# Performance work log

Hardware: AMD Instinct MI355X
Metric: run time of the kernel (lower is better)

The kernel has to match this reference:

```python
import jax, jax.numpy as jnp
import numpy as np

INPUT_SIZE = 512
HIDDEN = 512
LAYERS = 4
T = 256
B = 64


def _weight_size():
    total = 0
    for l in range(LAYERS):
        insize = INPUT_SIZE if l == 0 else HIDDEN
        total += insize * 6 * HIDDEN + HIDDEN * 5 * HIDDEN
    return total


def setup_inputs() -> dict:
    key = jax.random.key(0)
    k1, k2, k3 = jax.random.split(key, 3)
    inputs = jax.random.normal(k1, (B, T, INPUT_SIZE), dtype=jnp.float32)
    lengths = jax.random.randint(k2, (B,), T // 2, T + 1)
    lengths = jnp.sort(lengths)[::-1].astype(jnp.int32)  # descending, like pack_padded
    weight = jax.random.normal(k3, (_weight_size(),), dtype=jnp.float32) * 0.05
    # bias: zeros except forget-gate block (second of 5) filled with 1, per layer
    b_layer = jnp.concatenate([
        jnp.zeros((HIDDEN,), jnp.float32),
        jnp.ones((HIDDEN,), jnp.float32),
        jnp.zeros((3 * HIDDEN,), jnp.float32),
    ])
    bias = jnp.tile(b_layer, LAYERS)
    return {"inputs": inputs, "weight": weight, "bias": bias, "lengths": lengths}


def _split_params(weight, bias):
    params = []
    idx = 0
    for l in range(LAYERS):
        insize = INPUT_SIZE if l == 0 else HIDDEN
        n = insize * 6 * HIDDEN
        W_ih = weight[idx:idx + n].reshape(insize, 6 * HIDDEN); idx += n
        n = HIDDEN * 5 * HIDDEN
        W_hh = weight[idx:idx + n].reshape(HIDDEN, 5 * HIDDEN); idx += n
        b = bias[l * 5 * HIDDEN:(l + 1) * 5 * HIDDEN]
        params.append((W_ih, W_hh, b))
    return params


def _reverse_padded(x, lengths):
    # x: [T, B, D]; reverse each sequence within its own length, keep padding in place
    t = jnp.arange(x.shape[0])[:, None]                      # [T, 1]
    L = lengths[None, :]                                     # [1, B]
    idx = jnp.where(t < L, L - 1 - t, t)                     # [T, B]
    return jnp.take_along_axis(x, idx[:, :, None], axis=0)


def _run_layer(x, W_ih, W_hh, b, mask):
    # x: [T, B, D], mask: [T, B, 1] (1.0 where t < length)
    H = HIDDEN
    xi = jnp.einsum('tbd,dg->tbg', x, W_ih)                  # [T, B, 6H] (batched GEMM)

    def step(carry, inp):
        h, c = carry
        xi_t, m = inp
        g = xi_t[:, :5 * H] + h @ W_hh + b                   # [B, 5H]
        i = jax.nn.sigmoid(g[:, 0 * H:1 * H])
        f = jax.nn.sigmoid(g[:, 1 * H:2 * H])
        gc = jnp.tanh(g[:, 2 * H:3 * H])
        o = jax.nn.sigmoid(g[:, 3 * H:4 * H])
        r = jax.nn.sigmoid(g[:, 4 * H:5 * H])                # highway transform gate
        lin = xi_t[:, 5 * H:]                                # highway linear projection of input
        c_new = (f * c + i * gc) * m
        h_new = (r * (o * jnp.tanh(c_new)) + (1.0 - r) * lin) * m
        return (h_new, c_new), h_new

    h0 = jnp.zeros((x.shape[1], H), x.dtype)
    (_, _), hs = jax.lax.scan(step, (h0, h0), (xi, mask))
    return hs                                                # [T, B, H]


def reference(inputs, weight, bias, lengths):
    x = jnp.transpose(inputs, (1, 0, 2))                     # [T, B, D]
    mask = (jnp.arange(T)[:, None] < lengths[None, :]).astype(x.dtype)[:, :, None]
    x = x * mask                                             # emulate packed-sequence zero padding
    for l, (W_ih, W_hh, b) in enumerate(_split_params(weight, bias)):
        rev = (l % 2 == 1)                                   # layers alternate direction
        if rev:
            x = _reverse_padded(x, lengths)
        h = _run_layer(x, W_ih, W_hh, b, mask)
        if rev:
            h = _reverse_padded(h, lengths)
        x = h
    return jnp.transpose(x, (1, 0, 2))                       # [B, T, H]
```

## Files before the change

### kernel.cpp

```cpp
#include <hip/hip_runtime.h>
#include <hip/hip_bf16.h>

#define T_STEPS 256
#define BATCH 64
#define HID 512
#define GATES 3072
#define NLAYERS 4
#define BT_GROUPS 4
#define GBLK 32
#define SCAN_THREADS 256
#define HSTR 520
#define GLP 84

typedef __bf16 bf16_t;
typedef _Float16 fp16_t;
typedef __attribute__((ext_vector_type(8))) __bf16 bf16x8;
typedef __attribute__((ext_vector_type(4))) float f32x4;
typedef __attribute__((ext_vector_type(4))) unsigned int u32x4;

__device__ __forceinline__ float sigm(float x){ return 1.0f/(1.0f + __expf(-x)); }
__device__ __forceinline__ float tanh_f(float x){ return 2.0f/(1.0f + __expf(-2.0f*x)) - 1.0f; }
__device__ __forceinline__ unsigned short f2bf(float x){ __bf16 b=(__bf16)x; return __builtin_bit_cast(unsigned short, b); }

__global__ void transpose_cast_kernel(const float* __restrict__ src, unsigned short* __restrict__ dst, int R, int C){
  __shared__ float tile[32][33];
  int tx = threadIdx.x & 31, ty = threadIdx.x >> 5;
  int c0 = blockIdx.x*32, r0 = blockIdx.y*32;
  #pragma unroll
  for(int i=0;i<4;i++){ int r = r0 + ty + i*8; tile[ty+i*8][tx] = src[(size_t)r*C + c0 + tx]; }
  __syncthreads();
  #pragma unroll
  for(int i=0;i<4;i++){ int c = c0 + ty + i*8; dst[(size_t)c*R + r0 + tx] = f2bf(tile[tx][ty+i*8]); }
}

__global__ void prep_x0_kernel(const float* __restrict__ inp, const int* __restrict__ lens, unsigned short* __restrict__ x0){
  int idx = blockIdx.x*blockDim.x + threadIdx.x;
  int e = idx*4;
  int d = e & (HID-1);
  int tb = e >> 9;
  int b = tb & (BATCH-1);
  int t = tb >> 6;
  const float4 v = *(const float4*)(inp + ((size_t)b*T_STEPS + t)*HID + d);
  float m = (t < lens[b]) ? 1.f : 0.f;
  ushort4 u; u.x=f2bf(v.x*m); u.y=f2bf(v.y*m); u.z=f2bf(v.z*m); u.w=f2bf(v.w*m);
  *(ushort4*)(x0 + ((size_t)t*BATCH + b)*HID + d) = u;
}

__global__ void __launch_bounds__(256,2)
xi_gemm_kernel(const unsigned short* __restrict__ A,
               const unsigned short* __restrict__ BT,
               fp16_t* __restrict__ C)
{
  __shared__ __align__(16) unsigned short As[128*72];
  __shared__ __align__(16) unsigned short Bs[128*72];
  const int tid = threadIdx.x, lane = tid & 63, wv = tid >> 6;
  const int frow = lane & 15, quad = lane >> 4;
  const int m0 = blockIdx.x*128, n0 = blockIdx.y*128;
  const int mh = (wv>>1)*64, nh = (wv&1)*64;
  const int sr = tid>>1, sk = (tid&1)*32;
  f32x4 acc[4][4];
  #pragma unroll
  for(int mt=0;mt<4;mt++)
    #pragma unroll
    for(int nt=0;nt<4;nt++) acc[mt][nt] = (f32x4){0.f,0.f,0.f,0.f};

  for(int kc=0;kc<512;kc+=64){
    #pragma unroll
    for(int i=0;i<4;i++){
      *(uint4*)(As + sr*72 + sk + i*8) = *(const uint4*)(A + (size_t)(m0+sr)*512 + kc + sk + i*8);
      *(uint4*)(Bs + sr*72 + sk + i*8) = *(const uint4*)(BT + (size_t)(n0+sr)*512 + kc + sk + i*8);
    }
    __syncthreads();
    #pragma unroll
    for(int ks=0;ks<2;ks++){
      bf16x8 av[4], bv[4];
      #pragma unroll
      for(int mt=0;mt<4;mt++) av[mt] = *(const bf16x8*)(As + (mh+mt*16+frow)*72 + ks*32 + quad*8);
      #pragma unroll
      for(int nt=0;nt<4;nt++) bv[nt] = *(const bf16x8*)(Bs + (nh+nt*16+frow)*72 + ks*32 + quad*8);
      #pragma unroll
      for(int mt=0;mt<4;mt++)
        #pragma unroll
        for(int nt=0;nt<4;nt++)
          acc[mt][nt] = __builtin_amdgcn_mfma_f32_16x16x32_bf16(av[mt], bv[nt], acc[mt][nt],0,0,0);
    }
    __syncthreads();
  }
  #pragma unroll
  for(int mt=0;mt<4;mt++)
    #pragma unroll
    for(int nt=0;nt<4;nt++)
      #pragma unroll
      for(int r4=0;r4<4;r4++)
        C[(size_t)(m0+mh+mt*16+quad*4+r4)*GATES + n0+nh+nt*16+frow] = (fp16_t)acc[mt][nt][r4];
}

__global__ void __launch_bounds__(SCAN_THREADS,1)
scan_kernel(const fp16_t* __restrict__ Xi,
            const unsigned short* __restrict__ WhhT,
            const float* __restrict__ bias_l,
            const int* __restrict__ lens,
            unsigned short* __restrict__ Hxb,
            int* __restrict__ flags,
            unsigned short* __restrict__ xdst,
            float* __restrict__ dout,
            int rev)
{
  __shared__ __align__(16) unsigned short Al[16*HSTR];
  __shared__ float gl[64*GLP];
  __shared__ float bl[80];
  __shared__ int ll[16];
  __shared__ __align__(8) unsigned short hl[256];

  const int tid = threadIdx.x;
  const int bt  = blockIdx.x & (BT_GROUPS-1);
  const int g   = blockIdx.x >> 2;
  const int lane = tid & 63, wv = tid >> 6;
  const int frow = lane & 15, quad = lane >> 4;

  for(int i=tid;i<80;i+=SCAN_THREADS) bl[i] = bias_l[(i>>4)*HID + g*16 + (i&15)];
  if(tid<16) ll[tid] = lens[bt*16+tid];
  __syncthreads();

  bf16x8 Bf[5][4];
  #pragma unroll
  for(int q=0;q<5;q++)
    #pragma unroll
    for(int j=0;j<4;j++)
      Bf[q][j] = *(const bf16x8*)(WhhT + (size_t)(q*HID + g*16 + frow)*HID + (wv + j*4)*32 + quad*8);

  const int cr = tid >> 4;
  const int jj = tid & 15;
  const int brow_g = bt*16 + cr;
  const int hcol   = g*16 + jj;
  const int L_r = ll[cr];
  float cst=0.f, hs=0.f;
  unsigned short hbf=0; int tprev=0;

  for(int s=0; s<T_STEPS; s++){
    if(s>0){
      if(wv==0){
        int r = lane>>2, c4 = (lane&3)*4;
        unsigned long long v = *(const unsigned long long*)(hl + r*16 + c4);
        const unsigned short* dst = Hxb + (size_t)(s&1)*BATCH*HID + (size_t)(bt*16+r)*HID + g*16 + c4;
        asm volatile("global_store_dwordx2 %0, %1, off sc0 sc1" :: "v"(dst), "v"(v) : "memory");
        asm volatile("s_waitcnt vmcnt(0)" ::: "memory");
        if(lane==0)
          __hip_atomic_store(flags + bt*GBLK + g, s, __ATOMIC_RELAXED, __HIP_MEMORY_SCOPE_AGENT);
      }
      if(dout) dout[((size_t)brow_g*T_STEPS + tprev)*HID + hcol] = hs;
      else     xdst[((size_t)tprev*BATCH + brow_g)*HID + hcol] = hbf;
      if(wv==1){
        const int* fpp = flags + bt*GBLK + (lane & (GBLK-1));
        int it = 0;
        while(1){
          int v = __hip_atomic_load(fpp, __ATOMIC_RELAXED, __HIP_MEMORY_SCOPE_AGENT);
          if(__all(v >= s)) break;
          if(++it > (1<<20)) break;
        }
        asm volatile("" ::: "memory");
      }
    }
    __syncthreads();

    u32x4 hv[4];
    {
      const unsigned short* hbase = Hxb + (size_t)(s&1)*BATCH*HID + (size_t)bt*16*HID;
      #pragma unroll
      for(int i=0;i<4;i++){
        int idx = tid + i*256;
        const unsigned short* p = hbase + (size_t)(idx>>6)*HID + (idx&63)*8;
        asm volatile("global_load_dwordx4 %0, %1, off sc0 sc1" : "=v"(hv[i]) : "v"(p) : "memory");
      }
    }
    bool valid = s < L_r;
    int tcur = rev ? (valid ? (L_r-1-s) : s) : s;
    const fp16_t* xr = Xi + ((size_t)tcur*BATCH + brow_g)*GATES + hcol;
    fp16_t x0v=xr[0], x1v=xr[512], x2v=xr[1024], x3v=xr[1536], x4v=xr[2048], x5v=xr[2560];
    asm volatile("s_waitcnt vmcnt(0)" ::: "memory");
    #pragma unroll
    for(int i=0;i<4;i++){
      int idx = tid + i*256;
      *(u32x4*)(Al + (idx>>6)*HSTR + (idx&63)*8) = hv[i];
    }
    __syncthreads();

    f32x4 acc[5];
    #pragma unroll
    for(int q=0;q<5;q++) acc[q] = (f32x4){0.f,0.f,0.f,0.f};
    #pragma unroll
    for(int j=0;j<4;j++){
      bf16x8 a = *(const bf16x8*)((const bf16_t*)Al + (size_t)frow*HSTR + (wv + j*4)*32 + quad*8);
      #pragma unroll
      for(int q=0;q<5;q++)
        acc[q] = __builtin_amdgcn_mfma_f32_16x16x32_bf16(a, Bf[q][j], acc[q],0,0,0);
    }
    #pragma unroll
    for(int q=0;q<5;q++)
      #pragma unroll
      for(int r4=0;r4<4;r4++)
        gl[(wv*16 + quad*4 + r4)*GLP + q*16 + frow] = acc[q][r4];
    __syncthreads();

    {
      float ga[5];
      #pragma unroll
      for(int q=0;q<5;q++){
        float sum = bl[q*16+jj];
        #pragma unroll
        for(int w=0;w<4;w++) sum += gl[(w*16+cr)*GLP + q*16 + jj];
        ga[q] = sum;
      }
      ga[0] += (float)x0v; ga[1] += (float)x1v; ga[2] += (float)x2v;
      ga[3] += (float)x3v; ga[4] += (float)x4v;
      float m = valid ? 1.f : 0.f;
      float gi=sigm(ga[0]), gf=sigm(ga[1]), gcv=tanh_f(ga[2]), go=sigm(ga[3]), grv=sigm(ga[4]);
      cst = (gf*cst + gi*gcv) * m;
      hs  = (grv*(go*tanh_f(cst)) + (1.f-grv)*(float)x5v) * m;
      hbf = f2bf(hs);
      hl[cr*16+jj] = hbf;
      tprev = tcur;
    }
    __syncthreads();
  }

  if(dout) dout[((size_t)brow_g*T_STEPS + tprev)*HID + hcol] = hs;
  else     xdst[((size_t)tprev*BATCH + brow_g)*HID + hcol] = hbf;
}

extern "C" void kernel_launch(void* const* d_in, const int* in_sizes, int n_in,
                              void* d_out, int out_size, void* d_ws, size_t ws_size,
                              hipStream_t stream){
  const float* inp    = (const float*)d_in[0];
  const float* weight = (const float*)d_in[1];
  const float* bias   = (const float*)d_in[2];
  const int*   lens   = (const int*)d_in[3];
  float* dout = (float*)d_out;

  char* ws = (char*)d_ws;
  size_t off = 0;
  const size_t WTL = (size_t)(3072+2560)*512;
  unsigned short* WT = (unsigned short*)(ws+off); off += (size_t)NLAYERS*WTL*2;
  unsigned short* x0 = (unsigned short*)(ws+off); off += (size_t)T_STEPS*BATCH*HID*2;
  unsigned short* xA = (unsigned short*)(ws+off); off += (size_t)T_STEPS*BATCH*HID*2;
  fp16_t* Xi = (fp16_t*)(ws+off); off += (size_t)T_STEPS*BATCH*GATES*2;
  unsigned short* Hxb = (unsigned short*)(ws+off); off += (size_t)2*BATCH*HID*2;
  int* flags = (int*)(ws+off); off += 512;

  const size_t WS_L = (size_t)512*3072 + (size_t)512*2560;
  for(int l=0;l<NLAYERS;l++){
    const float* wih = weight + l*WS_L;
    const float* whh = wih + (size_t)512*3072;
    unsigned short* wihT = WT + l*WTL;
    unsigned short* whhT = wihT + (size_t)3072*512;
    transpose_cast_kernel<<<dim3(3072/32,512/32),256,0,stream>>>(wih, wihT, 512, 3072);
    transpose_cast_kernel<<<dim3(2560/32,512/32),256,0,stream>>>(whh, whhT, 512, 2560);
  }
  prep_x0_kernel<<<8192,256,0,stream>>>(inp, lens, x0);

  const unsigned short* bufs_in[4]  = {x0, xA, x0, xA};
  unsigned short*       bufs_out[4] = {xA, x0, xA, nullptr};
  for(int l=0;l<NLAYERS;l++){
    xi_gemm_kernel<<<dim3(128,24),256,0,stream>>>(bufs_in[l], WT + l*WTL, Xi);
    hipMemsetAsync(Hxb, 0, (size_t)2*BATCH*HID*2 + 512, stream);
    scan_kernel<<<BT_GROUPS*GBLK, SCAN_THREADS, 0, stream>>>(
        Xi, WT + l*WTL + (size_t)3072*512,
        bias + (size_t)l*2560, lens, Hxb, flags,
        bufs_out[l], (l==3) ? dout : nullptr, l&1);
  }
}
```

Before: 3.473 ms.

## Use sentinel-filled hidden-state sequence buffer as data-carried flag instead of flag polling

The per-step handoff between scan blocks changes. Each block now stores its packed bf16 h values straight into a full-time-step buffer pre-filled with 0xFF. Consumers spin-load the previous step's rows until no sentinel words remain, which replaces the separate flag store, drain wait, flag poll and extra barriers. For forward layers this buffer is also the layer output, which removes the separate output writes. The cost is a memset of the whole sequence buffer per layer, plus a small risk that a valid bf16 pair equals the sentinel bit pattern.

```diff
diff --git a/kernel.cpp b/kernel.cpp
--- a/kernel.cpp
+++ b/kernel.cpp
@@ -11,6 +11,7 @@
 #define SCAN_THREADS 256
 #define HSTR 520
 #define GLP 84
+#define POLL_VALVE 4096
 
 typedef __bf16 bf16_t;
 typedef _Float16 fp16_t;
@@ -100,8 +101,7 @@
             const unsigned short* __restrict__ WhhT,
             const float* __restrict__ bias_l,
             const int* __restrict__ lens,
-            unsigned short* __restrict__ Hxb,
-            int* __restrict__ flags,
+            unsigned short* __restrict__ Hseq,
             unsigned short* __restrict__ xdst,
             float* __restrict__ dout,
             int rev)
@@ -110,7 +110,6 @@
   __shared__ float gl[64*GLP];
   __shared__ float bl[80];
   __shared__ int ll[16];
-  __shared__ __align__(8) unsigned short hl[256];
 
   const int tid = threadIdx.x;
   const int bt  = blockIdx.x & (BT_GROUPS-1);
@@ -137,47 +136,53 @@
   float cst=0.f, hs=0.f;
   unsigned short hbf=0; int tprev=0;
 
+  const size_t pofs[4] = {
+    (size_t)((tid      )>>6)*HID + (size_t)((tid      )&63)*8,
+    (size_t)((tid+256  )>>6)*HID + (size_t)((tid+256  )&63)*8,
+    (size_t)((tid+512  )>>6)*HID + (size_t)((tid+512  )&63)*8,
+    (size_t)((tid+768  )>>6)*HID + (size_t)((tid+768  )&63)*8 };
+
   for(int s=0; s<T_STEPS; s++){
-    if(s>0){
-      if(wv==0){
-        int r = lane>>2, c4 = (lane&3)*4;
-        unsigned long long v = *(const unsigned long long*)(hl + r*16 + c4);
-        const unsigned short* dst = Hxb + (size_t)(s&1)*BATCH*HID + (size_t)(bt*16+r)*HID + g*16 + c4;
-        asm volatile("global_store_dwordx2 %0, %1, off sc0 sc1" :: "v"(dst), "v"(v) : "memory");
-        asm volatile("s_waitcnt vmcnt(0)" ::: "memory");
-        if(lane==0)
-          __hip_atomic_store(flags + bt*GBLK + g, s, __ATOMIC_RELAXED, __HIP_MEMORY_SCOPE_AGENT);
-      }
+    if(rev && s>0){
       if(dout) dout[((size_t)brow_g*T_STEPS + tprev)*HID + hcol] = hs;
       else     xdst[((size_t)tprev*BATCH + brow_g)*HID + hcol] = hbf;
-      if(wv==1){
-        const int* fpp = flags + bt*GBLK + (lane & (GBLK-1));
-        int it = 0;
-        while(1){
-          int v = __hip_atomic_load(fpp, __ATOMIC_RELAXED, __HIP_MEMORY_SCOPE_AGENT);
-          if(__all(v >= s)) break;
-          if(++it > (1<<20)) break;
-        }
-        asm volatile("" ::: "memory");
-      }
-    }
-    __syncthreads();
-
-    u32x4 hv[4];
-    {
-      const unsigned short* hbase = Hxb + (size_t)(s&1)*BATCH*HID + (size_t)bt*16*HID;
-      #pragma unroll
-      for(int i=0;i<4;i++){
-        int idx = tid + i*256;
-        const unsigned short* p = hbase + (size_t)(idx>>6)*HID + (idx&63)*8;
-        asm volatile("global_load_dwordx4 %0, %1, off sc0 sc1" : "=v"(hv[i]) : "v"(p) : "memory");
-      }
-    }
+    }
+
     bool valid = s < L_r;
     int tcur = rev ? (valid ? (L_r-1-s) : s) : s;
     const fp16_t* xr = Xi + ((size_t)tcur*BATCH + brow_g)*GATES + hcol;
     fp16_t x0v=xr[0], x1v=xr[512], x2v=xr[1024], x3v=xr[1536], x4v=xr[2048], x5v=xr[2560];
-    asm volatile("s_waitcnt vmcnt(0)" ::: "memory");
+
+    u32x4 hv[4];
+    if(s==0){
+      #pragma unroll
+      for(int i=0;i<4;i++) hv[i] = (u32x4){0u,0u,0u,0u};
+    } else {
+      const unsigned short* hb = Hseq + (size_t)(s-1)*BATCH*HID + (size_t)bt*16*HID;
+      int it = 0;
+      while(1){
+        #pragma unroll
+        for(int i=0;i<4;i++){
+          const unsigned short* p = hb + pofs[i];
+          asm volatile("global_load_dwordx4 %0, %1, off sc0 sc1" : "=v"(hv[i]) : "v"(p) : "memory");
+        }
+        asm volatile("s_waitcnt vmcnt(0)"
+                     : "+v"(hv[0]), "+v"(hv[1]), "+v"(hv[2]), "+v"(hv[3])
+                     :: "memory");
+        __builtin_amdgcn_sched_barrier(0);
+        unsigned int bad = 0u;
+        #pragma unroll
+        for(int i=0;i<4;i++){
+          bad |= (unsigned)(hv[i][0] == 0xFFFFFFFFu);
+          bad |= (unsigned)(hv[i][1] == 0xFFFFFFFFu);
+          bad |= (unsigned)(hv[i][2] == 0xFFFFFFFFu);
+          bad |= (unsigned)(hv[i][3] == 0xFFFFFFFFu);
+        }
+        if(!bad) break;
+        if(++it > POLL_VALVE) break;
+        __builtin_amdgcn_s_sleep(1);
+      }
+    }
     #pragma unroll
     for(int i=0;i<4;i++){
       int idx = tid + i*256;
@@ -218,14 +223,21 @@
       cst = (gf*cst + gi*gcv) * m;
       hs  = (grv*(go*tanh_f(cst)) + (1.f-grv)*(float)x5v) * m;
       hbf = f2bf(hs);
-      hl[cr*16+jj] = hbf;
       tprev = tcur;
-    }
-    __syncthreads();
-  }
-
-  if(dout) dout[((size_t)brow_g*T_STEPS + tprev)*HID + hcol] = hs;
-  else     xdst[((size_t)tprev*BATCH + brow_g)*HID + hcol] = hbf;
+
+      int up = __shfl_down((int)(unsigned int)hbf, 1);
+      if((jj&1)==0){
+        unsigned int packed = (unsigned int)hbf | (((unsigned int)up & 0xFFFFu) << 16);
+        unsigned int* dst = (unsigned int*)(Hseq + (size_t)s*BATCH*HID + (size_t)brow_g*HID + hcol);
+        asm volatile("global_store_dword %0, %1, off sc0 sc1" :: "v"(dst), "v"(packed) : "memory");
+      }
+    }
+  }
+
+  if(rev){
+    if(dout) dout[((size_t)brow_g*T_STEPS + tprev)*HID + hcol] = hs;
+    else     xdst[((size_t)tprev*BATCH + brow_g)*HID + hcol] = hbf;
+  }
 }
 
 extern "C" void kernel_launch(void* const* d_in, const int* in_sizes, int n_in,
@@ -244,8 +256,8 @@
   unsigned short* x0 = (unsigned short*)(ws+off); off += (size_t)T_STEPS*BATCH*HID*2;
   unsigned short* xA = (unsigned short*)(ws+off); off += (size_t)T_STEPS*BATCH*HID*2;
   fp16_t* Xi = (fp16_t*)(ws+off); off += (size_t)T_STEPS*BATCH*GATES*2;
-  unsigned short* Hxb = (unsigned short*)(ws+off); off += (size_t)2*BATCH*HID*2;
-  int* flags = (int*)(ws+off); off += 512;
+
+  const size_t HSEQ_BYTES = (size_t)T_STEPS*BATCH*HID*2;
 
   const size_t WS_L = (size_t)512*3072 + (size_t)512*2560;
   for(int l=0;l<NLAYERS;l++){
@@ -258,14 +270,16 @@
   }
   prep_x0_kernel<<<8192,256,0,stream>>>(inp, lens, x0);
 
-  const unsigned short* bufs_in[4]  = {x0, xA, x0, xA};
-  unsigned short*       bufs_out[4] = {xA, x0, xA, nullptr};
+  const unsigned short* gemm_in[4] = {x0, xA, x0, xA};
+  unsigned short*       hseq_l[4]  = {xA, xA, xA, x0};
+  unsigned short*       xdst_l[4]  = {nullptr, x0, nullptr, nullptr};
+
   for(int l=0;l<NLAYERS;l++){
-    xi_gemm_kernel<<<dim3(128,24),256,0,stream>>>(bufs_in[l], WT + l*WTL, Xi);
-    hipMemsetAsync(Hxb, 0, (size_t)2*BATCH*HID*2 + 512, stream);
+    xi_gemm_kernel<<<dim3(128,24),256,0,stream>>>(gemm_in[l], WT + l*WTL, Xi);
+    hipMemsetAsync(hseq_l[l], 0xFF, HSEQ_BYTES, stream);
     scan_kernel<<<BT_GROUPS*GBLK, SCAN_THREADS, 0, stream>>>(
         Xi, WT + l*WTL + (size_t)3072*512,
-        bias + (size_t)l*2560, lens, Hxb, flags,
-        bufs_out[l], (l==3) ? dout : nullptr, l&1);
-  }
-}
+        bias + (size_t)l*2560, lens, hseq_l[l],
+        xdst_l[l], (l==3) ? dout : nullptr, l&1);
+  }
+}
```

Result: faster. 3.063 ms (-11.8%).
